# Performance work log

Hardware: AMD Instinct MI355X
Metric: run time of the kernel (lower is better)

Reference implementation:

```python
import jax, jax.numpy as jnp
import numpy as np

D_MODEL, D_K, D_V, BLOCK = 1024, 128, 128, 2048
B, T = 8, 2048

def setup_inputs() -> dict:
    key = jax.random.key(0)
    kx, kq, kk, kv = jax.random.split(key, 4)
    # nn.Linear weights are [out_features, in_features]
    s = 1.0 / np.sqrt(D_MODEL)
    return {
        "x": jax.random.normal(kx, (B, T, D_MODEL), dtype=jnp.float32),
        "W_q": jax.random.uniform(kq, (D_K, D_MODEL), jnp.float32, -s, s),
        "W_k": jax.random.uniform(kk, (D_K, D_MODEL), jnp.float32, -s, s),
        "W_v": jax.random.uniform(kv, (D_V, D_MODEL), jnp.float32, -s, s),
    }

def reference(x, W_q, W_k, W_v) -> jnp.ndarray:
    Tlen = x.shape[1]
    Q = jnp.einsum('btc,kc->btk', x, W_q)   # [B,T,d_k]
    K = jnp.einsum('btc,kc->btk', x, W_k)   # [B,T,d_k]
    V = jnp.einsum('btc,vc->btv', x, W_v)   # [B,T,d_v]
    scores = jnp.einsum('bqk,bsk->bqs', Q, K) / jnp.sqrt(jnp.float32(D_K))
    causal = jnp.tril(jnp.ones((Tlen, Tlen), dtype=bool))[None, :, :]
    scores = jnp.where(causal, scores, jnp.finfo(scores.dtype).min)
    attn = jax.nn.softmax(scores, axis=-1)
    return jnp.einsum('bqs,bsv->bqv', attn, V)  # [B,T,d_v]
```

## Files before the change

### kernel.cpp

```cpp
#include <hip/hip_runtime.h>
#include <hip/hip_fp16.h>

typedef _Float16 half8  __attribute__((ext_vector_type(8)));
typedef _Float16 half4v __attribute__((ext_vector_type(4)));
typedef float    f32x4  __attribute__((ext_vector_type(4)));

#define MFMA_F16 __builtin_amdgcn_mfma_f32_16x16x32_f16

#define BAR_LDS() asm volatile("s_waitcnt lgkmcnt(0)\n\ts_barrier" ::: "memory")
#define BAR_VM()  asm volatile("s_waitcnt vmcnt(0)\n\ts_barrier" ::: "memory")

__device__ __forceinline__ unsigned pack_f16(float a, float b) {
    union { __fp16 h __attribute__((ext_vector_type(2))); unsigned u; } cv;
    cv.h = __builtin_amdgcn_cvt_pkrtz(a, b);
    return cv.u;
}

__device__ __forceinline__ void gload16(const void* g, void* l) {
    __builtin_amdgcn_global_load_lds((const __attribute__((address_space(1))) void*)g,
                                     (__attribute__((address_space(3))) void*)l, 16, 0, 0);
}

__global__ __launch_bounds__(256) void wconv_k(const float* __restrict__ wq,
                                               const float* __restrict__ wk,
                                               const float* __restrict__ wv,
                                               _Float16* __restrict__ wh) {
    int i = (blockIdx.x * 256 + threadIdx.x) * 8;
    const float* src; int off;
    if (i < 131072)      { src = wq; off = i; }
    else if (i < 262144) { src = wk; off = i - 131072; }
    else                 { src = wv; off = i - 262144; }
    float4 a = *(const float4*)(src + off);
    float4 b = *(const float4*)(src + off + 4);
    half8 h;
    h[0]=(_Float16)a.x; h[1]=(_Float16)a.y; h[2]=(_Float16)a.z; h[3]=(_Float16)a.w;
    h[4]=(_Float16)b.x; h[5]=(_Float16)b.y; h[6]=(_Float16)b.z; h[7]=(_Float16)b.w;
    *(half8*)(wh + i) = h;
}

__global__ __launch_bounds__(256, 4) void qkv_k(const float* __restrict__ x,
                                                const _Float16* __restrict__ wh,
                                                _Float16* __restrict__ qh,
                                                _Float16* __restrict__ kh,
                                                _Float16* __restrict__ vth) {
    __shared__ float xs[2][64 * 64];
    const int tid = threadIdx.x;
    const int w = tid >> 6, l = tid & 63;
    const int fr = l & 15, fq = l >> 4;
    const int bid = blockIdx.x;
    const int xcd = bid & 7;
    const int slot = bid >> 3;
    const int rb = (slot / 3) * 8 + xcd;
    const int cb = slot % 3;
    const int row0 = rb * 64;
    const int c0 = cb * 128 + w * 32;
    const int xwk = (fr & 7) << 4;

    int srow[4], scolB[4];
#pragma unroll
    for (int i = 0; i < 4; ++i) {
        int ob = i * 4096 + w * 1024 + l * 16;
        srow[i]  = ob >> 8;
        scolB[i] = (ob & 255) ^ ((srow[i] & 7) << 4);
    }
    const _Float16* wgb = wh + (c0 + fr) * 1024 + fq * 8;

    f32x4 acc[4][2] = {};
    half8 wf[2][2];

#define GLX(kt, bb) do {                                                                  \
    _Pragma("unroll")                                                                     \
    for (int i = 0; i < 4; ++i)                                                           \
        gload16(x + (row0 + srow[i]) * 1024 + (kt) * 64 + (scolB[i] >> 2),                \
                (char*)(&xs[bb][0]) + i * 4096 + w * 1024);                               \
    } while (0)

#pragma unroll
    for (int nf = 0; nf < 2; ++nf) wf[0][nf] = *(const half8*)(wgb + nf * 16384);
    GLX(0, 0);
    BAR_VM();
    GLX(1, 1);

    int cur = 0;
    for (int kt = 0; kt < 16; ++kt) {
#pragma unroll
        for (int s = 0; s < 2; ++s) {
            const int ss = kt * 2 + s;
            if (ss + 1 < 32) {
#pragma unroll
                for (int nf = 0; nf < 2; ++nf)
                    wf[(ss + 1) & 1][nf] = *(const half8*)(wgb + nf * 16384 + (ss + 1) * 32);
            }
            half8 af[4];
#pragma unroll
            for (int mf = 0; mf < 4; ++mf) {
                const char* rp = (const char*)(&xs[cur][0]) + (mf * 16 + fr) * 256;
                const int X = s * 128 + fq * 32;
                float4 a0 = *(const float4*)(rp + (X ^ xwk));
                float4 a1 = *(const float4*)(rp + ((X + 16) ^ xwk));
                union { unsigned u[4]; half8 h; } cv;
                cv.u[0] = pack_f16(a0.x, a0.y);
                cv.u[1] = pack_f16(a0.z, a0.w);
                cv.u[2] = pack_f16(a1.x, a1.y);
                cv.u[3] = pack_f16(a1.z, a1.w);
                af[mf] = cv.h;
            }
#pragma unroll
            for (int mf = 0; mf < 4; ++mf)
#pragma unroll
                for (int nf = 0; nf < 2; ++nf)
                    acc[mf][nf] = MFMA_F16(af[mf], wf[ss & 1][nf], acc[mf][nf], 0, 0, 0);
        }
        BAR_VM();
        if (kt + 2 < 16) GLX(kt + 2, cur);
        cur ^= 1;
    }
#undef GLX

#pragma unroll
    for (int nf = 0; nf < 2; ++nf) {
        int n0 = c0 + nf * 16 + fr;
#pragma unroll
        for (int mf = 0; mf < 4; ++mf) {
            int mb = row0 + mf * 16 + fq * 4;
            if (cb == 0) {
#pragma unroll
                for (int r = 0; r < 4; ++r) qh[(mb + r) * 128 + n0] = (_Float16)acc[mf][nf][r];
            } else if (cb == 1) {
#pragma unroll
                for (int r = 0; r < 4; ++r) kh[(mb + r) * 128 + (n0 - 128)] = (_Float16)acc[mf][nf][r];
            } else {
                half4v pv;
#pragma unroll
                for (int r = 0; r < 4; ++r) pv[r] = (_Float16)acc[mf][nf][r];
                int t = mb & 2047;
                int tl = t & 63;
                int tp = (t & ~63) | (tl & 35) | ((tl & 12) << 1) | ((tl & 16) >> 2);
                *(half4v*)(&vth[((mb >> 11) * 128 + (n0 - 256)) * 2048 + tp]) = pv;
            }
        }
    }
}

__global__ __launch_bounds__(512, 4) void attn_k(const _Float16* __restrict__ qh,
                                                 const _Float16* __restrict__ kh,
                                                 const _Float16* __restrict__ vth,
                                                 _Float16* __restrict__ part,
                                                 float* __restrict__ stats,
                                                 float* __restrict__ out) {
    __shared__ _Float16 ks[2][32 * 128];
    __shared__ _Float16 vs[2][128 * 32];

    int bid = blockIdx.x;
    int b = bid & 7;
    int u = bid >> 3;
    int qt, c;
    {
        int idx = u;
        qt = 0;
        for (;;) { int nc = (qt >> 1) + 1; if (idx < nc) break; idx -= nc; ++qt; }
        c = idx;
    }
    int j0 = c * 8;
    int jmax = 4 * qt + 4;
    int j1 = j0 + 8 < jmax ? j0 + 8 : jmax;

    int tid = threadIdx.x, w = tid >> 6, l = tid & 63;
    int fr = l & 15, fq = l >> 4;
    int xw = (fr & 7) << 4;
    int xv = (fr & 3) << 4;

    const int kr  = tid >> 4;
    const int kc  = (tid & 15) ^ (kr & 7);
    const int vdd = tid >> 2;
    const int vc  = (tid & 3) ^ (vdd & 3);

    half8 qf[4];
    const _Float16* qp = qh + ((b * 2048 + qt * 128 + w * 16 + fr) << 7);
#pragma unroll
    for (int cc = 0; cc < 4; ++cc) qf[cc] = *(const half8*)(qp + cc * 32 + fq * 8);

#define GLOAD_TILE(j, bb) do {                                                            \
    gload16(kh + (((b << 11) + ((j) << 5) + kr) << 7) + kc * 8, &ks[bb][0] + w * 512);    \
    gload16(vth + (((b << 7) + vdd) << 11) + ((j) << 5) + vc * 8, &vs[bb][0] + w * 512);  \
    } while (0)

    f32x4 acc[8] = {};
    float mrow = -1e30f, lrow = 0.0f;

    GLOAD_TILE(j0, 0);
    BAR_VM();
    if (j0 + 1 < j1) GLOAD_TILE(j0 + 1, 1);

    int cur = 0;
    for (int j = j0; j < j1; ++j) {
        const char* ksb = (const char*)(ks[cur]);
        const char* vsb = (const char*)(vs[cur]);

        f32x4 s[2] = {};
        __builtin_amdgcn_s_setprio(1);
#pragma unroll
        for (int n = 0; n < 2; ++n) {
            const char* krow = ksb + (n * 16 + fr) * 256;
#pragma unroll
            for (int cc = 0; cc < 4; ++cc) {
                half8 kf = *(const half8*)(krow + ((cc * 64 + fq * 16) ^ xw));
                s[n] = MFMA_F16(kf, qf[cc], s[n], 0, 0, 0);
            }
        }
        __builtin_amdgcn_s_setprio(0);
        const float sc = 0.088388347648318447f;
        if (j >= 4 * qt) {
            int koff = (j - 4 * qt) << 5;
            int qrow = w * 16 + fr;
#pragma unroll
            for (int n = 0; n < 2; ++n)
#pragma unroll
                for (int r = 0; r < 4; ++r) {
                    int kcol = koff + n * 16 + fq * 4 + r;
                    float v = s[n][r] * sc;
                    s[n][r] = (kcol > qrow) ? -1e30f : v;
                }
        } else {
#pragma unroll
            for (int n = 0; n < 2; ++n)
#pragma unroll
                for (int r = 0; r < 4; ++r) s[n][r] *= sc;
        }

        float pmax = s[0][0];
#pragma unroll
        for (int n = 0; n < 2; ++n)
#pragma unroll
            for (int r = 0; r < 4; ++r) pmax = fmaxf(pmax, s[n][r]);
        float al = 1.0f;
        if (!__all(pmax - mrow <= 8.0f)) {
            float mx = pmax;
            mx = fmaxf(mx, __shfl_xor(mx, 16));
            mx = fmaxf(mx, __shfl_xor(mx, 32));
            float nm = fmaxf(mrow, mx);
            al = __expf(mrow - nm);
            mrow = nm;
#pragma unroll
            for (int dt = 0; dt < 8; ++dt)
#pragma unroll
                for (int r = 0; r < 4; ++r) acc[dt][r] *= al;
        }
        float rs = 0.f;
#pragma unroll
        for (int n = 0; n < 2; ++n)
#pragma unroll
            for (int r = 0; r < 4; ++r) {
                float p = __expf(s[n][r] - mrow);
                s[n][r] = p;
                rs += p;
            }
        rs += __shfl_xor(rs, 16);
        rs += __shfl_xor(rs, 32);
        lrow = lrow * al + rs;

        union { unsigned u[4]; half8 h; } pb;
        pb.u[0] = pack_f16(s[0][0], s[0][1]);
        pb.u[1] = pack_f16(s[0][2], s[0][3]);
        pb.u[2] = pack_f16(s[1][0], s[1][1]);
        pb.u[3] = pack_f16(s[1][2], s[1][3]);

        __builtin_amdgcn_s_setprio(1);
#pragma unroll
        for (int dt = 0; dt < 8; ++dt) {
            const char* vrow = vsb + (dt * 16 + fr) * 64;
            half8 vf = *(const half8*)(vrow + ((fq * 16) ^ xv));
            acc[dt] = MFMA_F16(vf, pb.h, acc[dt], 0, 0, 0);
        }
        __builtin_amdgcn_s_setprio(0);

        BAR_VM();
        if (j + 2 < j1) GLOAD_TILE(j + 2, cur);
        cur ^= 1;
    }

    float inv = 1.0f / lrow;

    if (qt < 2) {
        float* op = out + ((b * 2048 + qt * 128 + w * 16 + fr) << 7) + fq * 4;
#pragma unroll
        for (int dt = 0; dt < 8; ++dt) {
            float4 o;
            o.x = acc[dt][0] * inv; o.y = acc[dt][1] * inv;
            o.z = acc[dt][2] * inv; o.w = acc[dt][3] * inv;
            *(float4*)(op + dt * 16) = o;
        }
    } else {
        _Float16* op = part + bid * 16384 + w * 2048 + l * 4;
#pragma unroll
        for (int dt = 0; dt < 8; ++dt) {
            half4v h;
#pragma unroll
            for (int r = 0; r < 4; ++r) h[r] = (_Float16)(acc[dt][r] * inv);
            *(half4v*)(op + dt * 256) = h;
        }
        if (l < 16) {
            int ridx = bid * 128 + w * 16 + l;
            float2 st; st.x = mrow; st.y = lrow;
            *(float2*)(&stats[ridx * 2]) = st;
        }
    }
#undef GLOAD_TILE
}

__global__ __launch_bounds__(256) void comb_k(const _Float16* __restrict__ part,
                                              const float* __restrict__ stats,
                                              float* __restrict__ out) {
    int bid = blockIdx.x;
    int b = bid & 7;
    int rest = bid >> 3;
    int qt = 2 + (rest >> 2);
    int rh = rest & 3;
    int h = qt >> 1;
    int nc = h + 1;
    int u0 = qt + h * (h - 1) + (qt & 1) * h;
    int t = threadIdx.x;
    int row = rh * 32 + (t >> 3), g = t & 7;
    int w = row >> 4, q16 = row & 15;

    float mstar = -1e30f, mv[8], lv[8];
#pragma unroll
    for (int cc = 0; cc < 8; ++cc) {
        if (cc < nc) {
            int sidx = (((u0 + cc) << 3) + b) * 128 + row;
            mv[cc] = stats[sidx * 2];
            lv[cc] = stats[sidx * 2 + 1];
            mstar = fmaxf(mstar, mv[cc]);
        }
    }
    float den = 0.f, wc[8];
#pragma unroll
    for (int cc = 0; cc < 8; ++cc) {
        if (cc < nc) { wc[cc] = __expf(mv[cc] - mstar) * lv[cc]; den += wc[cc]; }
        else wc[cc] = 0.f;
    }
    float a[16] = {};
#pragma unroll
    for (int cc = 0; cc < 8; ++cc) {
        if (cc < nc) {
            const _Float16* pp = part + ((((u0 + cc) << 3) + b) * 16384) + w * 2048 + g * 256;
            float wcc = wc[cc];
#pragma unroll
            for (int fq = 0; fq < 4; ++fq) {
                half4v hh = *(const half4v*)(pp + (fq * 16 + q16) * 4);
#pragma unroll
                for (int r = 0; r < 4; ++r)
                    a[fq * 4 + r] += wcc * (float)hh[r];
            }
        }
    }
    float id = 1.0f / den;
    float* op = out + (b * 2048 + qt * 128 + row) * 128 + g * 16;
#pragma unroll
    for (int uu = 0; uu < 4; ++uu) {
        float4 o;
        o.x = a[uu * 4]     * id;
        o.y = a[uu * 4 + 1] * id;
        o.z = a[uu * 4 + 2] * id;
        o.w = a[uu * 4 + 3] * id;
        *(float4*)(op + uu * 4) = o;
    }
}

extern "C" void kernel_launch(void* const* d_in, const int* in_sizes, int n_in,
                              void* d_out, int out_size, void* d_ws, size_t ws_size,
                              hipStream_t stream) {
    const float* x  = (const float*)d_in[0];
    const float* wq = (const float*)d_in[1];
    const float* wk = (const float*)d_in[2];
    const float* wv = (const float*)d_in[3];

    char* ws = (char*)d_ws;
    _Float16* wh   = (_Float16*)(ws);
    _Float16* qhp  = (_Float16*)(ws + (1u  << 20));
    _Float16* khp  = (_Float16*)(ws + (5u  << 20));
    _Float16* vtp  = (_Float16*)(ws + (9u  << 20));
    _Float16* part = (_Float16*)(ws + (13u << 20));
    float*    stat = (float*)   (ws + (32u << 20));

    wconv_k<<<192, 256, 0, stream>>>(wq, wk, wv, wh);
    qkv_k<<<768, 256, 0, stream>>>(x, wh, qhp, khp, vtp);
    attn_k<<<576, 512, 0, stream>>>(qhp, khp, vtp, part, stat, (float*)d_out);
    comb_k<<<448, 256, 0, stream>>>(part, stat, (float*)d_out);
}
```

Baseline: 78.94 us.

## Triple-buffer QKV projection staging x and weights through LDS with partial waits

Restructures the QKV projection GEMM loop into a three-stage LDS pipeline with a smaller k-step (32 instead of 64). Weight fragments are now staged into swizzled LDS by async global-to-LDS loads instead of being read per lane straight from global memory. The barrier waits with vmcnt(4), so the loads for the next stage can stay in flight during compute. Occupancy hint drops from 4 to 3 blocks per SM to make room for the extra LDS, and there are twice as many barriers per block.

```diff
diff --git a/kernel.cpp b/kernel.cpp
--- a/kernel.cpp
+++ b/kernel.cpp
@@ -7,8 +7,8 @@
 
 #define MFMA_F16 __builtin_amdgcn_mfma_f32_16x16x32_f16
 
-#define BAR_LDS() asm volatile("s_waitcnt lgkmcnt(0)\n\ts_barrier" ::: "memory")
-#define BAR_VM()  asm volatile("s_waitcnt vmcnt(0)\n\ts_barrier" ::: "memory")
+#define BAR_VM4() asm volatile("s_waitcnt vmcnt(4)\n\ts_barrier" ::: "memory")
+#define BAR_VM0() asm volatile("s_waitcnt vmcnt(0)\n\ts_barrier" ::: "memory")
 
 __device__ __forceinline__ unsigned pack_f16(float a, float b) {
     union { __fp16 h __attribute__((ext_vector_type(2))); unsigned u; } cv;
@@ -38,12 +38,13 @@
     *(half8*)(wh + i) = h;
 }
 
-__global__ __launch_bounds__(256, 4) void qkv_k(const float* __restrict__ x,
+__global__ __launch_bounds__(256, 3) void qkv_k(const float* __restrict__ x,
                                                 const _Float16* __restrict__ wh,
                                                 _Float16* __restrict__ qh,
                                                 _Float16* __restrict__ kh,
                                                 _Float16* __restrict__ vth) {
-    __shared__ float xs[2][64 * 64];
+    __shared__ float    xs[3][64 * 32];
+    __shared__ _Float16 wsb[3][128 * 32];
     const int tid = threadIdx.x;
     const int w = tid >> 6, l = tid & 63;
     const int fr = l & 15, fq = l >> 4;
@@ -54,68 +55,78 @@
     const int cb = slot % 3;
     const int row0 = rb * 64;
     const int c0 = cb * 128 + w * 32;
-    const int xwk = (fr & 7) << 4;
-
-    int srow[4], scolB[4];
-#pragma unroll
-    for (int i = 0; i < 4; ++i) {
-        int ob = i * 4096 + w * 1024 + l * 16;
-        srow[i]  = ob >> 8;
-        scolB[i] = (ob & 255) ^ ((srow[i] & 7) << 4);
-    }
-    const _Float16* wgb = wh + (c0 + fr) * 1024 + fq * 8;
+    const int xk = (fr & 7) << 4;
+
+    int xrow[2], xcol[2];
+#pragma unroll
+    for (int i = 0; i < 2; ++i) {
+        int ob = i * 4096 + tid * 16;
+        xrow[i] = ob >> 7;
+        xcol[i] = ((ob & 127) ^ ((xrow[i] & 7) << 4)) >> 2;
+    }
+    int wrow_[2], wcol_[2];
+#pragma unroll
+    for (int i = 0; i < 2; ++i) {
+        int ob = i * 4096 + tid * 16;
+        wrow_[i] = ob >> 6;
+        wcol_[i] = ((ob & 63) ^ ((wrow_[i] & 3) << 4)) >> 1;
+    }
 
     f32x4 acc[4][2] = {};
-    half8 wf[2][2];
-
-#define GLX(kt, bb) do {                                                                  \
+
+#define STAGE(kt, bb) do {                                                                \
     _Pragma("unroll")                                                                     \
-    for (int i = 0; i < 4; ++i)                                                           \
-        gload16(x + (row0 + srow[i]) * 1024 + (kt) * 64 + (scolB[i] >> 2),                \
-                (char*)(&xs[bb][0]) + i * 4096 + w * 1024);                               \
+    for (int i = 0; i < 2; ++i)                                                           \
+        gload16(x + (row0 + xrow[i]) * 1024 + (kt) * 32 + xcol[i],                        \
+                (char*)(&xs[bb][0]) + i * 4096 + tid * 16);                               \
+    _Pragma("unroll")                                                                     \
+    for (int i = 0; i < 2; ++i)                                                           \
+        gload16(wh + (cb * 128 + wrow_[i]) * 1024 + (kt) * 32 + wcol_[i],                 \
+                (char*)(&wsb[bb][0]) + i * 4096 + tid * 16);                              \
     } while (0)
 
-#pragma unroll
-    for (int nf = 0; nf < 2; ++nf) wf[0][nf] = *(const half8*)(wgb + nf * 16384);
-    GLX(0, 0);
-    BAR_VM();
-    GLX(1, 1);
-
-    int cur = 0;
-    for (int kt = 0; kt < 16; ++kt) {
-#pragma unroll
-        for (int s = 0; s < 2; ++s) {
-            const int ss = kt * 2 + s;
-            if (ss + 1 < 32) {
-#pragma unroll
-                for (int nf = 0; nf < 2; ++nf)
-                    wf[(ss + 1) & 1][nf] = *(const half8*)(wgb + nf * 16384 + (ss + 1) * 32);
-            }
-            half8 af[4];
-#pragma unroll
-            for (int mf = 0; mf < 4; ++mf) {
-                const char* rp = (const char*)(&xs[cur][0]) + (mf * 16 + fr) * 256;
-                const int X = s * 128 + fq * 32;
-                float4 a0 = *(const float4*)(rp + (X ^ xwk));
-                float4 a1 = *(const float4*)(rp + ((X + 16) ^ xwk));
-                union { unsigned u[4]; half8 h; } cv;
-                cv.u[0] = pack_f16(a0.x, a0.y);
-                cv.u[1] = pack_f16(a0.z, a0.w);
-                cv.u[2] = pack_f16(a1.x, a1.y);
-                cv.u[3] = pack_f16(a1.z, a1.w);
-                af[mf] = cv.h;
-            }
-#pragma unroll
-            for (int mf = 0; mf < 4; ++mf)
-#pragma unroll
-                for (int nf = 0; nf < 2; ++nf)
-                    acc[mf][nf] = MFMA_F16(af[mf], wf[ss & 1][nf], acc[mf][nf], 0, 0, 0);
-        }
-        BAR_VM();
-        if (kt + 2 < 16) GLX(kt + 2, cur);
-        cur ^= 1;
-    }
-#undef GLX
+    STAGE(0, 0);
+    STAGE(1, 1);
+
+    int rd = 0, stg = 2;
+    for (int kt = 0; kt < 32; ++kt) {
+        if (kt < 31) BAR_VM4();
+        else         BAR_VM0();
+        if (kt + 2 < 32) STAGE(kt + 2, stg);
+
+        const char* xb = (const char*)(&xs[rd][0]);
+        const char* wb = (const char*)(&wsb[rd][0]);
+        half8 af[4];
+#pragma unroll
+        for (int mf = 0; mf < 4; ++mf) {
+            const char* rp = xb + (mf * 16 + fr) * 128;
+            float4 a0 = *(const float4*)(rp + ((fq * 32) ^ xk));
+            float4 a1 = *(const float4*)(rp + ((fq * 32 + 16) ^ xk));
+            union { unsigned u[4]; half8 h; } cv;
+            cv.u[0] = pack_f16(a0.x, a0.y);
+            cv.u[1] = pack_f16(a0.z, a0.w);
+            cv.u[2] = pack_f16(a1.x, a1.y);
+            cv.u[3] = pack_f16(a1.z, a1.w);
+            af[mf] = cv.h;
+        }
+        half8 bf[2];
+#pragma unroll
+        for (int nf = 0; nf < 2; ++nf) {
+            int wr = w * 32 + nf * 16 + fr;
+            bf[nf] = *(const half8*)(wb + wr * 64 + ((fq * 16) ^ ((wr & 3) << 4)));
+        }
+        __builtin_amdgcn_s_setprio(1);
+#pragma unroll
+        for (int mf = 0; mf < 4; ++mf)
+#pragma unroll
+            for (int nf = 0; nf < 2; ++nf)
+                acc[mf][nf] = MFMA_F16(af[mf], bf[nf], acc[mf][nf], 0, 0, 0);
+        __builtin_amdgcn_s_setprio(0);
+
+        stg = rd;
+        rd = (rd == 2) ? 0 : rd + 1;
+    }
+#undef STAGE
 
 #pragma unroll
     for (int nf = 0; nf < 2; ++nf) {
@@ -142,6 +153,7 @@
     }
 }
 
+#define BAR_VMA() asm volatile("s_waitcnt vmcnt(0)\n\ts_barrier" ::: "memory")
 __global__ __launch_bounds__(512, 4) void attn_k(const _Float16* __restrict__ qh,
                                                  const _Float16* __restrict__ kh,
                                                  const _Float16* __restrict__ vth,
@@ -189,7 +201,7 @@
     float mrow = -1e30f, lrow = 0.0f;
 
     GLOAD_TILE(j0, 0);
-    BAR_VM();
+    BAR_VMA();
     if (j0 + 1 < j1) GLOAD_TILE(j0 + 1, 1);
 
     int cur = 0;
@@ -274,7 +286,7 @@
         }
         __builtin_amdgcn_s_setprio(0);
 
-        BAR_VM();
+        BAR_VMA();
         if (j + 2 < j1) GLOAD_TILE(j + 2, cur);
         cur ^= 1;
     }
```

New measurement: 72.21 us, median of 3. 8.5% less time.
